# Kernel optimization log

Measured on AMD Instinct MI355X. Metric: run time of the kernel, lower is better.

Reference implementation:

```python
import jax, jax.numpy as jnp
import numpy as np
from jax import lax

B, C, H, W = 256, 3, 224, 224
M_MAG = 9.0  # RandAugment magnitude (init arg m)


def setup_inputs() -> dict:
    key = jax.random.key(0)
    k1, k2 = jax.random.split(key)
    # CIFAR-style normalization constants (as in the source module)
    mean = jnp.array([0.4914, 0.4822, 0.4465], dtype=jnp.float32)
    std = jnp.array([0.2023, 0.1994, 0.201], dtype=jnp.float32)
    # raw image in [0,1], then normalized (module expects normalized input)
    img = jax.random.uniform(k1, (B, C, H, W), dtype=jnp.float32)
    x = (img - mean[None, :, None, None]) / std[None, :, None, None]
    return {"x": x, "mean": mean, "std": std}


def _forward(x, mean, std):
    # deterministic op chain: sharpness -> contrast -> brightness -> solarize
    v_blend = M_MAG / 30.0 * (1.9 - 0.1) + 0.1   # 0.64 for sharpness/contrast/brightness
    v_sol = M_MAG / 30.0 * 1.0                    # 0.3 solarize threshold
    m_ = mean[None, :, None, None]
    s_ = std[None, :, None, None]

    # denormalize
    y = x * s_ + m_

    # sharpness: blend with 3x3 blur (kernel [[1,1,1],[1,5,1],[1,1,1]]/13, zero pad)
    k = jnp.array([[1., 1., 1.], [1., 5., 1.], [1., 1., 1.]], dtype=y.dtype) / 13.0
    kern = jnp.broadcast_to(k[None, None], (3, 1, 3, 3))  # depthwise OIHW
    blur = lax.conv_general_dilated(
        y, kern, window_strides=(1, 1), padding=[(1, 1), (1, 1)],
        feature_group_count=3, dimension_numbers=("NCHW", "OIHW", "NCHW"))
    y = y * v_blend + blur * (1.0 - v_blend)

    # contrast: blend with per-image mean of grayscale
    gray = 0.299 * y[:, 0] + 0.587 * y[:, 1] + 0.114 * y[:, 2]  # [B,H,W]
    gm = gray.mean(axis=(1, 2))[:, None, None, None]             # [B,1,1,1]
    y = y * v_blend + gm * (1.0 - v_blend)

    # brightness: blend with zeros
    y = y * v_blend

    # solarize: invert pixels >= threshold
    y = jnp.where(y < v_sol, y, 1.0 - y)

    # normalize
    return (y - m_) / s_


def reference(x, mean, std):
    return _forward(x, mean, std)
```

## Files before the change

### kernel.cpp

```cpp
#include <hip/hip_runtime.h>

#define IMG_B 256
#define IMG_H 224
#define IMG_W 224
#define HWPIX 50176
#define YP 228

#define FA(a,b) __fadd_rn((a),(b))
#define FM(a,b) __fmul_rn((a),(b))
#define FS(a,b) __fsub_rn((a),(b))
#define FD(a,b) __fdiv_rn((a),(b))

typedef float nt4 __attribute__((ext_vector_type(4)));

__device__ __forceinline__ float VBF()   { return (float)(9.0/30.0*(1.9-0.1)+0.1); }
__device__ __forceinline__ float OMVBF() { return (float)(1.0 - (9.0/30.0*(1.9-0.1)+0.1)); }
__device__ __forceinline__ float VSF()   { return (float)(9.0/30.0*1.0); }

__device__ __forceinline__ void y1_from_rows(const float* yU, const float* yC,
                                             const float* yD, float* y1o) {
    const float WN = 1.0f / 13.0f, WC = 5.0f / 13.0f;
#pragma unroll
    for (int mm = 0; mm < 4; ++mm) {
        float acc = 0.0f;
        acc = FA(acc, FM(WN, yU[mm + 0]));
        acc = FA(acc, FM(WN, yU[mm + 1]));
        acc = FA(acc, FM(WN, yU[mm + 2]));
        acc = FA(acc, FM(WN, yC[mm + 0]));
        acc = FA(acc, FM(WC, yC[mm + 1]));
        acc = FA(acc, FM(WN, yC[mm + 2]));
        acc = FA(acc, FM(WN, yD[mm + 0]));
        acc = FA(acc, FM(WN, yD[mm + 1]));
        acc = FA(acc, FM(WN, yD[mm + 2]));
        y1o[mm] = FA(FM(yC[mm + 1], VBF()), FM(acc, OMVBF()));
    }
}

__device__ __forceinline__ void stage_load(const float* __restrict__ xc, int r0,
                                           int t, float4* pf) {
#pragma unroll
    for (int u = 0; u < 4; ++u) {
        const int idx = t + 256 * u;
        float4 v = make_float4(0.f, 0.f, 0.f, 0.f);
        if (idx < 896) {
            const int row = idx / 56, c4 = (idx % 56) * 4;
            const int gi = r0 - 1 + row;
            if (gi >= 0 && gi < IMG_H)
                v = *(const float4*)(xc + (size_t)gi * IMG_W + c4);
        }
        pf[u] = v;
    }
}

__device__ __forceinline__ void stage_write(float s, float m, int r0, int t,
                                            const float4* pf, float* __restrict__ Y,
                                            int P) {
#pragma unroll
    for (int u = 0; u < 4; ++u) {
        const int idx = t + 256 * u;
        if (idx < 896) {
            const int row = idx / 56, c4 = (idx % 56) * 4;
            const int gi = r0 - 1 + row;
            float4 w;
            if (gi >= 0 && gi < IMG_H) {
                w.x = FA(FM(pf[u].x, s), m);
                w.y = FA(FM(pf[u].y, s), m);
                w.z = FA(FM(pf[u].z, s), m);
                w.w = FA(FM(pf[u].w, s), m);
            } else {
                w.x = w.y = w.z = w.w = 0.0f;
            }
            *(float4*)(&Y[row * P + c4]) = w;
        }
    }
}

__device__ __forceinline__ void lds_y6(const float* __restrict__ r, int j, float* y6) {
    const float4 vC = *(const float4*)(r + j);
    const float4 vL = *(const float4*)(r + (j > 0 ? j - 4 : 0));
    const float4 vR = *(const float4*)(r + (j + 4 < IMG_W ? j + 4 : IMG_W - 4));
    y6[0] = (j > 0) ? vL.w : 0.0f;
    y6[1] = vC.x; y6[2] = vC.y; y6[3] = vC.z; y6[4] = vC.w;
    y6[5] = (j + 4 < IMG_W) ? vR.x : 0.0f;
}

__global__ __launch_bounds__(256, 4) void kA1(const float* __restrict__ x,
                                              const float* __restrict__ mean_,
                                              const float* __restrict__ std_,
                                              float* __restrict__ part) {
    const int swz = (blockIdx.x & 7) * 512 + (blockIdx.x >> 3);
    const int ck = swz & 15, b = swz >> 4;
    const int t = threadIdx.x;
    const int r0 = ck * 14;

    __shared__ float SM[3648];
    float* Y  = SM;
    float* G2 = SM;
    float* CH = SM + 3328;

    const int rg  = t / 56;
    const int col = t - rg * 56;
    const bool active = (t < 224);
    const int rcount = (rg < 2) ? 4 : 3;
    const int rstart = (rg < 2) ? rg * 4 : 8 + (rg - 2) * 3;
    const int jd = col * 4;
    const bool lwave = ((t & 63) == 0)  && (col > 0);
    const bool rwave = ((t & 63) == 63) && (col < 55);

    const float s0 = std_[0], s1 = std_[1], s2 = std_[2];
    const float m0 = mean_[0], m1 = mean_[1], m2 = mean_[2];
    const float C0 = 0.299f, C1 = 0.587f, C2 = 0.114f;

    float4 q0[4], q1[4], q2[4];
#pragma unroll
    for (int u = 0; u < 4; ++u) {
        const int idx = t + 256 * u;
        q0[u] = q1[u] = q2[u] = make_float4(0.f, 0.f, 0.f, 0.f);
        if (idx < 896) {
            const int row = idx / 56, c4 = (idx % 56) * 4;
            const int gi = r0 - 1 + row;
            if (gi >= 0 && gi < IMG_H) {
                const float* p = x + (size_t)b * 3 * HWPIX + (size_t)gi * IMG_W + c4;
                q0[u] = *(const float4*)(p);
                q1[u] = *(const float4*)(p + HWPIX);
                q2[u] = *(const float4*)(p + 2 * HWPIX);
            }
        }
    }
#define GRAY1(a0v, a1v, a2v)                                              \
    FA(FA(FM(C0, FA(FM(a0v, s0), m0)), FM(C1, FA(FM(a1v, s1), m1))),      \
       FM(C2, FA(FM(a2v, s2), m2)))
#pragma unroll
    for (int u = 0; u < 4; ++u) {
        const int idx = t + 256 * u;
        if (idx < 896) {
            const int row = idx / 56, c4 = (idx % 56) * 4;
            const int gi = r0 - 1 + row;
            float4 w = make_float4(0.f, 0.f, 0.f, 0.f);
            if (gi >= 0 && gi < IMG_H) {
                w.x = GRAY1(q0[u].x, q1[u].x, q2[u].x);
                w.y = GRAY1(q0[u].y, q1[u].y, q2[u].y);
                w.z = GRAY1(q0[u].z, q1[u].z, q2[u].z);
                w.w = GRAY1(q0[u].w, q1[u].w, q2[u].w);
            }
            *(float4*)(&Y[row * YP + c4]) = w;
        }
    }
#undef GRAY1
    __syncthreads();

#define LOADROW(V, LWv, RWv, yr) do {                                 \
        V   = *(const float4*)(&Y[(yr) * YP + jd]);                   \
        LWv = __shfl_up(V.w, 1, 64);                                  \
        RWv = __shfl_down(V.x, 1, 64);                                \
        if (lwave) LWv = Y[(yr) * YP + jd - 1];                       \
        if (rwave) RWv = Y[(yr) * YP + jd + 4];                       \
    } while (0)

#define FILL6(y6, V, LWv, RWv) do {                                   \
        y6[0] = (col > 0) ? LWv : 0.0f;                               \
        y6[1] = V.x; y6[2] = V.y; y6[3] = V.z; y6[4] = V.w;           \
        y6[5] = (col < 55) ? RWv : 0.0f;                              \
    } while (0)

    float4 gacc[4];

    if (active) {
        float4 v0, v1, v2;
        float la0, la1, la2, ra0, ra1, ra2;
        LOADROW(v0, la0, ra0, rstart);
        LOADROW(v1, la1, ra1, rstart + 1);
#pragma unroll
        for (int k = 0; k < 4; ++k) {
            if (k < rcount) {
                LOADROW(v2, la2, ra2, rstart + k + 2);
                float yU[6], yC[6], yD[6], y1g[4];
                FILL6(yU, v0, la0, ra0);
                FILL6(yC, v1, la1, ra1);
                FILL6(yD, v2, la2, ra2);
                y1_from_rows(yU, yC, yD, y1g);
                gacc[k].x = y1g[0]; gacc[k].y = y1g[1];
                gacc[k].z = y1g[2]; gacc[k].w = y1g[3];
                v0 = v1; la0 = la1; ra0 = ra1;
                v1 = v2; la1 = la2; ra1 = ra2;
            }
        }
    }
    __syncthreads();

    if (active) {
#pragma unroll
        for (int k = 0; k < 4; ++k) {
            if (k < rcount) {
                const int pl = (rstart + k) * IMG_W + jd;
                const int grp = pl / 392;
                const int rem = pl - grp * 392;
                int li = rem / 96; if (li > 3) li = 3;
                const int o = rem - 96 * li;
                *(float4*)(&G2[(grp * 4 + li) * 104 + o]) = gacc[k];
            }
        }
    }
    __syncthreads();

    {
        const int leaf = t >> 3, e = t & 7;
        const int base = leaf * 104 + e;
        const int nk = ((leaf & 3) == 3) ? 13 : 12;
        float r = G2[base];
        for (int k = 1; k < nk; ++k) r = FA(r, G2[base + 8 * k]);
        CH[t] = r;
    }
    __syncthreads();

    if (t < 32) {
        const float* c8 = &CH[t * 8];
        float vv = FA(FA(FA(c8[0], c8[1]), FA(c8[2], c8[3])),
                      FA(FA(c8[4], c8[5]), FA(c8[6], c8[7])));
#pragma unroll
        for (int n = 16; n >= 1; n >>= 1) {
            const float lo = __shfl(vv, 2 * t, 64);
            const float hi = __shfl(vv, 2 * t + 1, 64);
            vv = FA(lo, hi);
        }
        if (t == 0) part[swz] = vv;
    }
#undef LOADROW
#undef FILL6
}

__global__ __launch_bounds__(256) void kB(const float* __restrict__ x,
                                          const float* __restrict__ mean_,
                                          const float* __restrict__ std_,
                                          const float* __restrict__ part,
                                          float* __restrict__ out) {
    const int swz = ((int)blockIdx.x & 7) * 1536 + ((int)blockIdx.x >> 3);
    const int ck = swz & 15;
    const int r1 = swz >> 4;
    const int c  = r1 % 3;
    const int b  = r1 / 3;
    const int t  = threadIdx.x;
    const int r0 = ck * 14;

    __shared__ float Y[16 * IMG_W];
    __shared__ float gsh;

    const float s = std_[c], m = mean_[c];
    float4 pf[4];
    stage_load(x + (size_t)(b * 3 + c) * HWPIX, r0, t, pf);

    if (t == 0) {
        float v[16];
#pragma unroll
        for (int k = 0; k < 16; ++k) v[k] = part[b * 16 + k];
#pragma unroll
        for (int n = 8; n >= 1; n >>= 1)
#pragma unroll
            for (int k = 0; k < 8; ++k)
                if (k < n) v[k] = FA(v[2 * k], v[2 * k + 1]);
        gsh = FD(v[0], 50176.0f);
    }

    stage_write(s, m, r0, t, pf, Y, IMG_W);
    __syncthreads();
    const float g = gsh;

    float* oc = out + (size_t)(b * 3 + c) * HWPIX + (size_t)r0 * IMG_W;

    for (int qi = t; qi < 784; qi += 256) {
        const int lr = qi / 56 + 1, j = (qi % 56) * 4;
        float yU[6], yC[6], yD[6], y1[4];
        lds_y6(&Y[(lr - 1) * IMG_W], j, yU);
        lds_y6(&Y[lr * IMG_W],       j, yC);
        lds_y6(&Y[(lr + 1) * IMG_W], j, yD);
        y1_from_rows(yU, yC, yD, y1);

        nt4 o4;
#pragma unroll
        for (int mm = 0; mm < 4; ++mm) {
            const float y2 = FA(FM(y1[mm], VBF()), FM(g, OMVBF()));
            const float y3 = FM(y2, VBF());
            const float y4 = (y3 < VSF()) ? y3 : FS(1.0f, y3);
            o4[mm] = FD(FS(y4, m), s);
        }
        __builtin_nontemporal_store(o4, (nt4*)(oc + (size_t)(lr - 1) * IMG_W + j));
    }
}

extern "C" void kernel_launch(void* const* d_in, const int* in_sizes, int n_in,
                              void* d_out, int out_size, void* d_ws, size_t ws_size,
                              hipStream_t stream) {
    const float* x     = (const float*)d_in[0];
    const float* mean_ = (const float*)d_in[1];
    const float* std_  = (const float*)d_in[2];
    float* out = (float*)d_out;

    float* part = (float*)d_ws;

    kA1<<<IMG_B * 16, 256, 0, stream>>>(x, mean_, std_, part);

    kB<<<IMG_B * 3 * 16, 256, 0, stream>>>(x, mean_, std_, part, out);
}
```

Measured before the change: 76.76 us.

## Split kA1 row chunks in half to double blocks and raise occupancy

```diff
diff --git a/kernel.cpp b/kernel.cpp
--- a/kernel.cpp
+++ b/kernel.cpp
@@ -84,25 +84,25 @@
     y6[5] = (j + 4 < IMG_W) ? vR.x : 0.0f;
 }
 
-__global__ __launch_bounds__(256, 4) void kA1(const float* __restrict__ x,
+__global__ __launch_bounds__(256, 8) void kA1(const float* __restrict__ x,
                                               const float* __restrict__ mean_,
                                               const float* __restrict__ std_,
                                               float* __restrict__ part) {
-    const int swz = (blockIdx.x & 7) * 512 + (blockIdx.x >> 3);
-    const int ck = swz & 15, b = swz >> 4;
+    const int swz = ((int)blockIdx.x & 7) * 1024 + ((int)blockIdx.x >> 3);
+    const int ck = swz & 31, b = swz >> 5;
     const int t = threadIdx.x;
-    const int r0 = ck * 14;
-
-    __shared__ float SM[3648];
+    const int r0 = ck * 7;
+
+    __shared__ float SM[2052];
     float* Y  = SM;
     float* G2 = SM;
-    float* CH = SM + 3328;
+    float* CH = SM + 1664;
 
     const int rg  = t / 56;
     const int col = t - rg * 56;
     const bool active = (t < 224);
-    const int rcount = (rg < 2) ? 4 : 3;
-    const int rstart = (rg < 2) ? rg * 4 : 8 + (rg - 2) * 3;
+    const int rcount = (rg < 3) ? 2 : 1;
+    const int rstart = rg * 2;
     const int jd = col * 4;
     const bool lwave = ((t & 63) == 0)  && (col > 0);
     const bool rwave = ((t & 63) == 63) && (col < 55);
@@ -111,37 +111,26 @@
     const float m0 = mean_[0], m1 = mean_[1], m2 = mean_[2];
     const float C0 = 0.299f, C1 = 0.587f, C2 = 0.114f;
 
-    float4 q0[4], q1[4], q2[4];
-#pragma unroll
-    for (int u = 0; u < 4; ++u) {
-        const int idx = t + 256 * u;
-        q0[u] = q1[u] = q2[u] = make_float4(0.f, 0.f, 0.f, 0.f);
-        if (idx < 896) {
-            const int row = idx / 56, c4 = (idx % 56) * 4;
-            const int gi = r0 - 1 + row;
-            if (gi >= 0 && gi < IMG_H) {
-                const float* p = x + (size_t)b * 3 * HWPIX + (size_t)gi * IMG_W + c4;
-                q0[u] = *(const float4*)(p);
-                q1[u] = *(const float4*)(p + HWPIX);
-                q2[u] = *(const float4*)(p + 2 * HWPIX);
-            }
-        }
-    }
 #define GRAY1(a0v, a1v, a2v)                                              \
     FA(FA(FM(C0, FA(FM(a0v, s0), m0)), FM(C1, FA(FM(a1v, s1), m1))),      \
        FM(C2, FA(FM(a2v, s2), m2)))
-#pragma unroll
-    for (int u = 0; u < 4; ++u) {
+
+#pragma unroll
+    for (int u = 0; u < 2; ++u) {
         const int idx = t + 256 * u;
-        if (idx < 896) {
+        if (idx < 504) {
             const int row = idx / 56, c4 = (idx % 56) * 4;
             const int gi = r0 - 1 + row;
             float4 w = make_float4(0.f, 0.f, 0.f, 0.f);
             if (gi >= 0 && gi < IMG_H) {
-                w.x = GRAY1(q0[u].x, q1[u].x, q2[u].x);
-                w.y = GRAY1(q0[u].y, q1[u].y, q2[u].y);
-                w.z = GRAY1(q0[u].z, q1[u].z, q2[u].z);
-                w.w = GRAY1(q0[u].w, q1[u].w, q2[u].w);
+                const float* p = x + (size_t)b * 3 * HWPIX + (size_t)gi * IMG_W + c4;
+                const float4 qa = *(const float4*)(p);
+                const float4 qb = *(const float4*)(p + HWPIX);
+                const float4 qc = *(const float4*)(p + 2 * HWPIX);
+                w.x = GRAY1(qa.x, qb.x, qc.x);
+                w.y = GRAY1(qa.y, qb.y, qc.y);
+                w.z = GRAY1(qa.z, qb.z, qc.z);
+                w.w = GRAY1(qa.w, qb.w, qc.w);
             }
             *(float4*)(&Y[row * YP + c4]) = w;
         }
@@ -163,7 +152,7 @@
         y6[5] = (col < 55) ? RWv : 0.0f;                              \
     } while (0)
 
-    float4 gacc[4];
+    float4 gacc[2];
 
     if (active) {
         float4 v0, v1, v2;
@@ -171,7 +160,7 @@
         LOADROW(v0, la0, ra0, rstart);
         LOADROW(v1, la1, ra1, rstart + 1);
 #pragma unroll
-        for (int k = 0; k < 4; ++k) {
+        for (int k = 0; k < 2; ++k) {
             if (k < rcount) {
                 LOADROW(v2, la2, ra2, rstart + k + 2);
                 float yU[6], yC[6], yD[6], y1g[4];
@@ -190,7 +179,7 @@
 
     if (active) {
 #pragma unroll
-        for (int k = 0; k < 4; ++k) {
+        for (int k = 0; k < 2; ++k) {
             if (k < rcount) {
                 const int pl = (rstart + k) * IMG_W + jd;
                 const int grp = pl / 392;
@@ -203,7 +192,7 @@
     }
     __syncthreads();
 
-    {
+    if (t < 128) {
         const int leaf = t >> 3, e = t & 7;
         const int base = leaf * 104 + e;
         const int nk = ((leaf & 3) == 3) ? 13 : 12;
@@ -213,12 +202,12 @@
     }
     __syncthreads();
 
-    if (t < 32) {
+    if (t < 16) {
         const float* c8 = &CH[t * 8];
         float vv = FA(FA(FA(c8[0], c8[1]), FA(c8[2], c8[3])),
                       FA(FA(c8[4], c8[5]), FA(c8[6], c8[7])));
 #pragma unroll
-        for (int n = 16; n >= 1; n >>= 1) {
+        for (int n = 8; n >= 1; n >>= 1) {
             const float lo = __shfl(vv, 2 * t, 64);
             const float hi = __shfl(vv, 2 * t + 1, 64);
             vv = FA(lo, hi);
@@ -250,13 +239,13 @@
     stage_load(x + (size_t)(b * 3 + c) * HWPIX, r0, t, pf);
 
     if (t == 0) {
-        float v[16];
-#pragma unroll
-        for (int k = 0; k < 16; ++k) v[k] = part[b * 16 + k];
-#pragma unroll
-        for (int n = 8; n >= 1; n >>= 1)
-#pragma unroll
-            for (int k = 0; k < 8; ++k)
+        float v[32];
+#pragma unroll
+        for (int k = 0; k < 32; ++k) v[k] = part[b * 32 + k];
+#pragma unroll
+        for (int n = 16; n >= 1; n >>= 1)
+#pragma unroll
+            for (int k = 0; k < 16; ++k)
                 if (k < n) v[k] = FA(v[2 * k], v[2 * k + 1]);
         gsh = FD(v[0], 50176.0f);
     }
@@ -297,7 +286,7 @@
 
     float* part = (float*)d_ws;
 
-    kA1<<<IMG_B * 16, 256, 0, stream>>>(x, mean_, std_, part);
+    kA1<<<IMG_B * 32, 256, 0, stream>>>(x, mean_, std_, part);
 
     kB<<<IMG_B * 3 * 16, 256, 0, stream>>>(x, mean_, std_, part, out);
 }
```

After: 75.65 us. Within noise of the previous version (-1.4%).
